# Kernel tuning notes

Hardware: AMD Instinct MI355X
Metric: run time of the kernel (lower is better)

## Reference

```python
import jax, jax.numpy as jnp
import numpy as np

N_NODES = 100000
N_EDGES = 2000000
EPS = 1e-8


def setup_inputs() -> dict:
    key = jax.random.key(0)
    k1, k2 = jax.random.split(key)
    node_positions = jax.random.normal(k1, (1, N_NODES, 2), dtype=jnp.float32) * 10.0
    adjacency = jnp.zeros((1, 1, 1), dtype=jnp.float32)  # unused by this axiom
    edge_index = jax.random.randint(k2, (2, N_EDGES), 0, N_NODES, dtype=jnp.int32)
    return {"node_positions": node_positions, "adjacency": adjacency, "edge_index": edge_index}


def reference(node_positions, adjacency, edge_index):
    """OrthogonalIntegrityAxiom loss.

    Mathematically identical to enumerating all intra-node edge pairs (i<j)
    and averaging cos^2(theta)*(1-cos^2(theta)) = dot^2 - dot^4 over pairs.
    Uses the moment identity: per node n with incident unit directions d_i,
      sum_{i,j} (d_i.d_j)^2 = ||sum_i d_i (x) d_i||_F^2
      sum_{i,j} (d_i.d_j)^4 = ||sum_i d_i^{(x)4}||_F^2
    Diagonal (i=j) terms equal 1 in both sums and cancel in the difference,
    so sum_{i<j} (dot^2 - dot^4) = (S2_n - S4_n)/2.
    """
    pos = node_positions.reshape(-1, 2)                      # (N, 2)
    n_total = pos.shape[0]
    src, dst = edge_index[0], edge_index[1]
    d = pos[dst] - pos[src]                                  # (E, 2)
    d = d / jnp.maximum(jnp.linalg.norm(d, axis=-1, keepdims=True), EPS)

    # Each edge is incident to both endpoints -> 2E (node, direction) pairs.
    nodes = jnp.concatenate([src, dst])                      # (2E,)
    dirs = jnp.concatenate([d, d], axis=0)                   # (2E, 2)

    o2 = (dirs[:, :, None] * dirs[:, None, :]).reshape(-1, 4)    # d (x) d, (2E, 4)
    o4 = (o2[:, :, None] * o2[:, None, :]).reshape(-1, 16)       # d^{(x)4}, (2E, 16)

    M = jax.ops.segment_sum(o2, nodes, num_segments=n_total)     # (N, 4)
    T = jax.ops.segment_sum(o4, nodes, num_segments=n_total)     # (N, 16)
    deg = jax.ops.segment_sum(jnp.ones_like(dirs[:, 0]), nodes, num_segments=n_total)

    S2 = jnp.sum(M * M, axis=-1)   # per-node sum_{i,j} (d_i.d_j)^2
    S4 = jnp.sum(T * T, axis=-1)   # per-node sum_{i,j} (d_i.d_j)^4

    pair_loss_sum = 0.5 * jnp.sum(S2 - S4)
    n_pairs = 0.5 * jnp.sum(deg * (deg - 1.0))
    loss = pair_loss_sum / jnp.maximum(n_pairs, 1.0)
    return loss
```

## Files before the change

### kernel.cpp

```cpp
#include <hip/hip_runtime.h>
#include <math.h>

#define EPSV 1e-8f

static constexpr double QC = 1.0 / 1024.0;
static constexpr double QS = 1.0 / 512.0;

static constexpr int BLOG = 8;
static constexpr int NPB = 1 << BLOG;
static constexpr int NBIN = 512;
static constexpr int SRTN = 8192;
static constexpr int NODE_BLOCKS = 256;

__device__ __forceinline__ unsigned int make_record(float dx, float dy) {
    float n2 = dx * dx + dy * dy;
    if (n2 > EPSV * EPSV) {
        float inv = 1.0f / n2;
        float c2 = (dx * dx - dy * dy) * inv;
        float s2 = (2.0f * dx * dy) * inv;
        float c4 = c2 * c2 - s2 * s2;
        float s4 = 2.0f * c2 * s2;
        c4 = fminf(fmaxf(c4, -1.0f), 1.0f);
        s4 = fminf(fmaxf(s4, -1.0f), 1.0f);
        unsigned int c4q = (unsigned int)__float2int_rn((c4 + 1.0f) * 1024.0f);
        unsigned int s4q = (unsigned int)__float2int_rn((s4 + 1.0f) * 512.0f);
        return (c4q << 11) | s4q;
    }
    return (1u << 31) | (1024u << 11) | 512u;
}

__device__ __forceinline__ unsigned long long rec_to_val(unsigned int r) {
    return (((unsigned long long)(r >> 31)) << 60) | (1ull << 52)
         | (((unsigned long long)((r >> 11) & 0xFFFu)) << 26)
         | (unsigned long long)(r & 0x7FFu);
}

__device__ __forceinline__ void decode_accum(unsigned long long a, double& pls, double& npr) {
    double s4sum = (double)(a & 0x3FFFFFFull);
    double c4sum = (double)((a >> 26) & 0x3FFFFFFull);
    double deg = (double)((a >> 52) & 0xFFull);
    double z = (double)(a >> 60);
    double u = deg - z;
    double C = c4sum * QC - deg;
    double S = s4sum * QS - deg;
    pls += (u * u - C * C - S * S) * 0.0625;
    npr += 0.5 * deg * (deg - 1.0);
}

__global__ __launch_bounds__(256) void bin_kernel(
    const float2* __restrict__ pos,
    const int* __restrict__ ei,
    int E, int NB, int chunk, int rstride,
    unsigned short* __restrict__ ofs_out,
    unsigned int* __restrict__ buf)
{
    __shared__ unsigned int srt[SRTN];
    __shared__ unsigned int hist[512];
    __shared__ unsigned int scan[512];
    int blk = blockIdx.x;
    int t = threadIdx.x;
    int e0 = blk * chunk;
    int e1 = min(E, e0 + chunk);
    int cl = max(0, e1 - e0);
    const int* src = ei;
    const int* dst = ei + E;

    hist[t] = 0; hist[t + 256] = 0;
    __syncthreads();
    for (int e = e0 + t; e < e1; e += 256) {
        atomicAdd(&hist[src[e] >> BLOG], 1u);
        atomicAdd(&hist[dst[e] >> BLOG], 1u);
    }
    __syncthreads();
    scan[t] = hist[t]; scan[t + 256] = hist[t + 256];
    __syncthreads();
    for (int d = 1; d < 512; d <<= 1) {
        unsigned a0 = scan[t] + ((t >= d) ? scan[t - d] : 0u);
        int t2 = t + 256;
        unsigned a1 = scan[t2] + ((t2 >= d) ? scan[t2 - d] : 0u);
        __syncthreads();
        scan[t] = a0; scan[t2] = a1;
        __syncthreads();
    }
    unsigned ex0 = scan[t] - hist[t];
    unsigned ex1 = scan[t + 256] - hist[t + 256];
    size_t row = (size_t)blk * (size_t)(NB + 1);
    if (t < NB) ofs_out[row + t] = (unsigned short)ex0;
    if (t + 256 < NB) ofs_out[row + t + 256] = (unsigned short)ex1;
    if (t == 0) ofs_out[row + NB] = (unsigned short)(2 * cl);
    __syncthreads();
    hist[t] = ex0; hist[t + 256] = ex1;
    __syncthreads();
    for (int e = e0 + t; e < e1; e += 256) {
        int s = src[e], d = dst[e];
        float2 ps = pos[s], pd = pos[d];
        unsigned int rec = make_record(pd.x - ps.x, pd.y - ps.y);
        unsigned is = atomicAdd(&hist[s >> BLOG], 1u);
        srt[is] = rec | ((unsigned)(s & (NPB - 1)) << 23);
        unsigned it = atomicAdd(&hist[d >> BLOG], 1u);
        srt[it] = rec | ((unsigned)(d & (NPB - 1)) << 23);
    }
    __syncthreads();
    unsigned int* dstb = buf + (size_t)blk * (size_t)rstride;
    int nrec = 2 * cl;
    for (int i = t; i < nrec; i += 256) dstb[i] = srt[i];
}

__global__ __launch_bounds__(512) void bucket_kernel(
    const unsigned int* __restrict__ buf,
    const unsigned short* __restrict__ ofs,
    int rstride, int NB, int nbin,
    double* __restrict__ partials)
{
    __shared__ unsigned long long acc[8][NPB];
    __shared__ unsigned int so0[NBIN], so1[NBIN];
    __shared__ double sha[8], shb[8];
    int b = blockIdx.x;
    int t = threadIdx.x;
    int wid = t >> 6;
    for (int i = t; i < 8 * NPB; i += 512)
        ((unsigned long long*)acc)[i] = 0ull;
    if (t < nbin) {
        size_t row = (size_t)t * (size_t)(NB + 1);
        so0[t] = ofs[row + b];
        so1[t] = ofs[row + b + 1];
    }
    __syncthreads();

    int g = t >> 4;
    int l = t & 15;
    for (int rr = g; rr < nbin; rr += 32) {
        unsigned o0 = so0[rr], o1 = so1[rr];
        const unsigned int* p = buf + (size_t)rr * (size_t)rstride;
        for (unsigned i = o0 + l; i < o1; i += 16) {
            unsigned r = p[i];
            unsigned id = (r >> 23) & (NPB - 1);
            atomicAdd(&acc[wid][id], rec_to_val(r));
        }
    }
    __syncthreads();

    double pls = 0.0, npr = 0.0;
    for (int i = t; i < NPB; i += 512) {
        unsigned long long a = 0ull;
        #pragma unroll
        for (int w = 0; w < 8; ++w) a += acc[w][i];
        decode_accum(a, pls, npr);
    }
    for (int off = 32; off > 0; off >>= 1) {
        pls += __shfl_down(pls, off, 64);
        npr += __shfl_down(npr, off, 64);
    }
    int lane = t & 63;
    if (lane == 0) { sha[wid] = pls; shb[wid] = npr; }
    __syncthreads();
    if (t == 0) {
        double a = 0.0, c = 0.0;
        #pragma unroll
        for (int w = 0; w < 8; ++w) { a += sha[w]; c += shb[w]; }
        partials[2 * b + 0] = a;
        partials[2 * b + 1] = c;
    }
}

__global__ __launch_bounds__(256) void final_kernel(
    const double* __restrict__ partials,
    float* __restrict__ out,
    int nb)
{
    double pls = 0.0, npr = 0.0;
    for (int i = threadIdx.x; i < nb; i += blockDim.x) {
        pls += partials[2 * i + 0];
        npr += partials[2 * i + 1];
    }
    __shared__ double sha[4], shb[4];
    for (int off = 32; off > 0; off >>= 1) {
        pls += __shfl_down(pls, off, 64);
        npr += __shfl_down(npr, off, 64);
    }
    int lane = threadIdx.x & 63;
    int wid = threadIdx.x >> 6;
    if (lane == 0) { sha[wid] = pls; shb[wid] = npr; }
    __syncthreads();
    if (threadIdx.x == 0) {
        double a = sha[0] + sha[1] + sha[2] + sha[3];
        double b = shb[0] + shb[1] + shb[2] + shb[3];
        out[0] = (float)(a / fmax(b, 1.0));
    }
}

__global__ __launch_bounds__(256) void edge_kernel_fb(
    const float2* __restrict__ pos,
    const int* __restrict__ ei,
    unsigned long long* __restrict__ acc,
    int E)
{
    int tid = blockIdx.x * blockDim.x + threadIdx.x;
    int nthreads = gridDim.x * blockDim.x;
    const int* src = ei;
    const int* dst = ei + E;
    for (int e = tid; e < E; e += nthreads) {
        int s = src[e], t = dst[e];
        float2 ps = pos[s], pt = pos[t];
        unsigned long long val = rec_to_val(make_record(pt.x - ps.x, pt.y - ps.y));
        atomicAdd(&acc[s], val);
        atomicAdd(&acc[t], val);
    }
}

__global__ __launch_bounds__(256) void node_kernel_fb(
    const unsigned long long* __restrict__ acc,
    double* __restrict__ partials,
    int N)
{
    int tid = blockIdx.x * blockDim.x + threadIdx.x;
    int nthreads = gridDim.x * blockDim.x;
    double pls = 0.0, npr = 0.0;
    for (int n = tid; n < N; n += nthreads)
        decode_accum(acc[n], pls, npr);
    __shared__ double sha[4], shb[4];
    for (int off = 32; off > 0; off >>= 1) {
        pls += __shfl_down(pls, off, 64);
        npr += __shfl_down(npr, off, 64);
    }
    int lane = threadIdx.x & 63;
    int wid = threadIdx.x >> 6;
    if (lane == 0) { sha[wid] = pls; shb[wid] = npr; }
    __syncthreads();
    if (threadIdx.x == 0) {
        partials[2 * blockIdx.x + 0] = sha[0] + sha[1] + sha[2] + sha[3];
        partials[2 * blockIdx.x + 1] = shb[0] + shb[1] + shb[2] + shb[3];
    }
}

extern "C" void kernel_launch(void* const* d_in, const int* in_sizes, int n_in,
                              void* d_out, int out_size, void* d_ws, size_t ws_size,
                              hipStream_t stream) {
    const float* pos = (const float*)d_in[0];
    const int* ei = (const int*)d_in[2];
    int N = in_sizes[0] / 2;
    int E = in_sizes[2] / 2;
    float* out = (float*)d_out;

    int NB = (N + NPB - 1) >> BLOG;
    int chunk = (E + NBIN - 1) / NBIN;
    int nrec_max = 2 * chunk;
    int rstride = (nrec_max + 15) & ~15;

    size_t off_buf = (size_t)NB * 16;
    size_t off_ofs = off_buf + (size_t)NBIN * (size_t)rstride * 4;
    size_t need = off_ofs + (size_t)NBIN * (size_t)(NB + 1) * 2;

    if (ws_size >= need && nrec_max <= SRTN && NB + 1 <= 512 && nrec_max < 65536) {
        double* partials = (double*)d_ws;
        unsigned int* buf = (unsigned int*)((char*)d_ws + off_buf);
        unsigned short* ofs = (unsigned short*)((char*)d_ws + off_ofs);

        bin_kernel<<<NBIN, 256, 0, stream>>>(
            (const float2*)pos, ei, E, NB, chunk, rstride, ofs, buf);
        bucket_kernel<<<NB, 512, 0, stream>>>(buf, ofs, rstride, NB, NBIN, partials);
        final_kernel<<<1, 256, 0, stream>>>(partials, out, NB);
    } else {
        unsigned long long* acc = (unsigned long long*)d_ws;
        double* partials = (double*)((char*)d_ws + (size_t)N * 8);
        hipMemsetAsync(d_ws, 0, (size_t)N * 8 + (size_t)NODE_BLOCKS * 16, stream);
        int eb = min((E + 255) / 256, 2048);
        edge_kernel_fb<<<eb, 256, 0, stream>>>((const float2*)pos, ei, acc, E);
        node_kernel_fb<<<NODE_BLOCKS, 256, 0, stream>>>(acc, partials, N);
        final_kernel<<<1, 256, 0, stream>>>(partials, out, NODE_BLOCKS);
    }
}
```

Measured before the change: 115.3 us.

## Compute edge records during histogram pass and fuse final reduction into bucket kernel

Edge direction records are now computed in the first histogram pass and kept in a shared-memory buffer, so the scatter pass no longer re-gathers positions. The final single-block reduction kernel is removed. Bucket blocks instead accumulate their partial sums with double atomics into a header that bin_kernel zeroes, and the last block to arrive writes the output. This saves a kernel launch and some redundant gathers, at the cost of extra LDS per block (which may lower occupancy), a non-deterministic summation order, and a last-block-done counter protocol.

```diff
diff --git a/kernel.cpp b/kernel.cpp
--- a/kernel.cpp
+++ b/kernel.cpp
@@ -10,6 +10,7 @@
 static constexpr int NPB = 1 << BLOG;
 static constexpr int NBIN = 512;
 static constexpr int SRTN = 8192;
+static constexpr int CHMAX = SRTN / 2;
 static constexpr int NODE_BLOCKS = 256;
 
 __device__ __forceinline__ unsigned int make_record(float dx, float dy) {
@@ -52,13 +53,16 @@
     const int* __restrict__ ei,
     int E, int NB, int chunk, int rstride,
     unsigned short* __restrict__ ofs_out,
-    unsigned int* __restrict__ buf)
+    unsigned int* __restrict__ buf,
+    unsigned long long* __restrict__ hdr)
 {
     __shared__ unsigned int srt[SRTN];
+    __shared__ unsigned int recbuf[CHMAX];
     __shared__ unsigned int hist[512];
     __shared__ unsigned int scan[512];
     int blk = blockIdx.x;
     int t = threadIdx.x;
+    if (blk == 0 && t < 4) hdr[t] = 0ull;
     int e0 = blk * chunk;
     int e1 = min(E, e0 + chunk);
     int cl = max(0, e1 - e0);
@@ -68,8 +72,11 @@
     hist[t] = 0; hist[t + 256] = 0;
     __syncthreads();
     for (int e = e0 + t; e < e1; e += 256) {
-        atomicAdd(&hist[src[e] >> BLOG], 1u);
-        atomicAdd(&hist[dst[e] >> BLOG], 1u);
+        int s = src[e], d = dst[e];
+        atomicAdd(&hist[s >> BLOG], 1u);
+        atomicAdd(&hist[d >> BLOG], 1u);
+        float2 ps = pos[s], pd = pos[d];
+        recbuf[e - e0] = make_record(pd.x - ps.x, pd.y - ps.y);
     }
     __syncthreads();
     scan[t] = hist[t]; scan[t + 256] = hist[t + 256];
@@ -93,8 +100,7 @@
     __syncthreads();
     for (int e = e0 + t; e < e1; e += 256) {
         int s = src[e], d = dst[e];
-        float2 ps = pos[s], pd = pos[d];
-        unsigned int rec = make_record(pd.x - ps.x, pd.y - ps.y);
+        unsigned int rec = recbuf[e - e0];
         unsigned is = atomicAdd(&hist[s >> BLOG], 1u);
         srt[is] = rec | ((unsigned)(s & (NPB - 1)) << 23);
         unsigned it = atomicAdd(&hist[d >> BLOG], 1u);
@@ -110,7 +116,8 @@
     const unsigned int* __restrict__ buf,
     const unsigned short* __restrict__ ofs,
     int rstride, int NB, int nbin,
-    double* __restrict__ partials)
+    unsigned long long* __restrict__ hdr,
+    float* __restrict__ out)
 {
     __shared__ unsigned long long acc[8][NPB];
     __shared__ unsigned int so0[NBIN], so1[NBIN];
@@ -158,8 +165,17 @@
         double a = 0.0, c = 0.0;
         #pragma unroll
         for (int w = 0; w < 8; ++w) { a += sha[w]; c += shb[w]; }
-        partials[2 * b + 0] = a;
-        partials[2 * b + 1] = c;
+        double* gs = (double*)hdr;
+        double r0 = atomicAdd(&gs[0], a);
+        double r1 = atomicAdd(&gs[1], c);
+        asm volatile("" :: "v"(r0), "v"(r1));
+        __threadfence();
+        unsigned long long cnt = atomicAdd(&hdr[2], 1ull);
+        if (cnt == (unsigned long long)(gridDim.x - 1)) {
+            double ta = atomicAdd(&gs[0], 0.0);
+            double tb = atomicAdd(&gs[1], 0.0);
+            out[0] = (float)(ta / fmax(tb, 1.0));
+        }
     }
 }
 
@@ -247,19 +263,18 @@
     int nrec_max = 2 * chunk;
     int rstride = (nrec_max + 15) & ~15;
 
-    size_t off_buf = (size_t)NB * 16;
+    size_t off_buf = 64;
     size_t off_ofs = off_buf + (size_t)NBIN * (size_t)rstride * 4;
     size_t need = off_ofs + (size_t)NBIN * (size_t)(NB + 1) * 2;
 
-    if (ws_size >= need && nrec_max <= SRTN && NB + 1 <= 512 && nrec_max < 65536) {
-        double* partials = (double*)d_ws;
+    if (ws_size >= need && chunk <= CHMAX && NB + 1 <= 512 && nrec_max < 65536) {
+        unsigned long long* hdr = (unsigned long long*)d_ws;
         unsigned int* buf = (unsigned int*)((char*)d_ws + off_buf);
         unsigned short* ofs = (unsigned short*)((char*)d_ws + off_ofs);
 
         bin_kernel<<<NBIN, 256, 0, stream>>>(
-            (const float2*)pos, ei, E, NB, chunk, rstride, ofs, buf);
-        bucket_kernel<<<NB, 512, 0, stream>>>(buf, ofs, rstride, NB, NBIN, partials);
-        final_kernel<<<1, 256, 0, stream>>>(partials, out, NB);
+            (const float2*)pos, ei, E, NB, chunk, rstride, ofs, buf, hdr);
+        bucket_kernel<<<NB, 512, 0, stream>>>(buf, ofs, rstride, NB, NBIN, hdr, out);
     } else {
         unsigned long long* acc = (unsigned long long*)d_ws;
         double* partials = (double*)((char*)d_ws + (size_t)N * 8);
```

Result: slower. 122.5 us (+6.3%).

## Stage edge indices in LDS with vectorized loads and widen bin kernel to 512 threads

Applied to the files above, without the earlier changes.

The bin kernel now reads each block's edge indices once with int4 loads into LDS (sdu/sdv) and builds its histogram from them. The scatter pass reuses these staged indices instead of re-reading global memory. Block size goes from 256 to 512 threads, the scan becomes one element per thread, and the final copy-out uses uint4 stores. The chunk is rounded to a multiple of 8 for alignment, and LDS use grows by 32KB per block, which may lower occupancy.

```diff
diff --git a/kernel.cpp b/kernel.cpp
--- a/kernel.cpp
+++ b/kernel.cpp
@@ -10,6 +10,7 @@
 static constexpr int NPB = 1 << BLOG;
 static constexpr int NBIN = 512;
 static constexpr int SRTN = 8192;
+static constexpr int SDMAX = 4096;
 static constexpr int NODE_BLOCKS = 256;
 
 __device__ __forceinline__ unsigned int make_record(float dx, float dy) {
@@ -47,14 +48,16 @@
     npr += 0.5 * deg * (deg - 1.0);
 }
 
-__global__ __launch_bounds__(256) void bin_kernel(
+__global__ __launch_bounds__(512) void bin_kernel(
     const float2* __restrict__ pos,
     const int* __restrict__ ei,
     int E, int NB, int chunk, int rstride,
     unsigned short* __restrict__ ofs_out,
     unsigned int* __restrict__ buf)
 {
-    __shared__ unsigned int srt[SRTN];
+    __shared__ __align__(16) unsigned int srt[SRTN];
+    __shared__ __align__(16) int sdu[SDMAX];
+    __shared__ __align__(16) int sdv[SDMAX];
     __shared__ unsigned int hist[512];
     __shared__ unsigned int scan[512];
     int blk = blockIdx.x;
@@ -62,37 +65,53 @@
     int e0 = blk * chunk;
     int e1 = min(E, e0 + chunk);
     int cl = max(0, e1 - e0);
-    const int* src = ei;
-    const int* dst = ei + E;
-
-    hist[t] = 0; hist[t + 256] = 0;
-    __syncthreads();
-    for (int e = e0 + t; e < e1; e += 256) {
-        atomicAdd(&hist[src[e] >> BLOG], 1u);
-        atomicAdd(&hist[dst[e] >> BLOG], 1u);
-    }
-    __syncthreads();
-    scan[t] = hist[t]; scan[t + 256] = hist[t + 256];
+    const int* src = ei + e0;
+    const int* dst = ei + E + e0;
+
+    hist[t] = 0;
+    __syncthreads();
+    if (((E & 3) == 0)) {
+        int nq = cl >> 2;
+        for (int q = t; q < nq; q += 512) {
+            int4 s4 = ((const int4*)src)[q];
+            int4 d4 = ((const int4*)dst)[q];
+            ((int4*)sdu)[q] = s4;
+            ((int4*)sdv)[q] = d4;
+            atomicAdd(&hist[s4.x >> BLOG], 1u);
+            atomicAdd(&hist[s4.y >> BLOG], 1u);
+            atomicAdd(&hist[s4.z >> BLOG], 1u);
+            atomicAdd(&hist[s4.w >> BLOG], 1u);
+            atomicAdd(&hist[d4.x >> BLOG], 1u);
+            atomicAdd(&hist[d4.y >> BLOG], 1u);
+            atomicAdd(&hist[d4.z >> BLOG], 1u);
+            atomicAdd(&hist[d4.w >> BLOG], 1u);
+        }
+    } else {
+        for (int i = t; i < cl; i += 512) {
+            int s = src[i], d = dst[i];
+            sdu[i] = s; sdv[i] = d;
+            atomicAdd(&hist[s >> BLOG], 1u);
+            atomicAdd(&hist[d >> BLOG], 1u);
+        }
+    }
+    __syncthreads();
+    scan[t] = hist[t];
     __syncthreads();
     for (int d = 1; d < 512; d <<= 1) {
-        unsigned a0 = scan[t] + ((t >= d) ? scan[t - d] : 0u);
-        int t2 = t + 256;
-        unsigned a1 = scan[t2] + ((t2 >= d) ? scan[t2 - d] : 0u);
+        unsigned a = scan[t] + ((t >= d) ? scan[t - d] : 0u);
         __syncthreads();
-        scan[t] = a0; scan[t2] = a1;
+        scan[t] = a;
         __syncthreads();
     }
-    unsigned ex0 = scan[t] - hist[t];
-    unsigned ex1 = scan[t + 256] - hist[t + 256];
+    unsigned ex = scan[t] - hist[t];
     size_t row = (size_t)blk * (size_t)(NB + 1);
-    if (t < NB) ofs_out[row + t] = (unsigned short)ex0;
-    if (t + 256 < NB) ofs_out[row + t + 256] = (unsigned short)ex1;
+    if (t < NB) ofs_out[row + t] = (unsigned short)ex;
     if (t == 0) ofs_out[row + NB] = (unsigned short)(2 * cl);
     __syncthreads();
-    hist[t] = ex0; hist[t + 256] = ex1;
-    __syncthreads();
-    for (int e = e0 + t; e < e1; e += 256) {
-        int s = src[e], d = dst[e];
+    hist[t] = ex;
+    __syncthreads();
+    for (int i = t; i < cl; i += 512) {
+        int s = sdu[i], d = sdv[i];
         float2 ps = pos[s], pd = pos[d];
         unsigned int rec = make_record(pd.x - ps.x, pd.y - ps.y);
         unsigned is = atomicAdd(&hist[s >> BLOG], 1u);
@@ -103,7 +122,13 @@
     __syncthreads();
     unsigned int* dstb = buf + (size_t)blk * (size_t)rstride;
     int nrec = 2 * cl;
-    for (int i = t; i < nrec; i += 256) dstb[i] = srt[i];
+    if ((nrec & 3) == 0) {
+        int nv = nrec >> 2;
+        for (int i = t; i < nv; i += 512)
+            ((uint4*)dstb)[i] = ((const uint4*)srt)[i];
+    } else {
+        for (int i = t; i < nrec; i += 512) dstb[i] = srt[i];
+    }
 }
 
 __global__ __launch_bounds__(512) void bucket_kernel(
@@ -243,7 +268,7 @@
     float* out = (float*)d_out;
 
     int NB = (N + NPB - 1) >> BLOG;
-    int chunk = (E + NBIN - 1) / NBIN;
+    int chunk = ((E + NBIN - 1) / NBIN + 7) & ~7;
     int nrec_max = 2 * chunk;
     int rstride = (nrec_max + 15) & ~15;
 
@@ -251,12 +276,13 @@
     size_t off_ofs = off_buf + (size_t)NBIN * (size_t)rstride * 4;
     size_t need = off_ofs + (size_t)NBIN * (size_t)(NB + 1) * 2;
 
-    if (ws_size >= need && nrec_max <= SRTN && NB + 1 <= 512 && nrec_max < 65536) {
+    if (ws_size >= need && chunk <= SDMAX && nrec_max <= SRTN
+        && NB + 1 <= 512 && nrec_max < 65536) {
         double* partials = (double*)d_ws;
         unsigned int* buf = (unsigned int*)((char*)d_ws + off_buf);
         unsigned short* ofs = (unsigned short*)((char*)d_ws + off_ofs);
 
-        bin_kernel<<<NBIN, 256, 0, stream>>>(
+        bin_kernel<<<NBIN, 512, 0, stream>>>(
             (const float2*)pos, ei, E, NB, chunk, rstride, ofs, buf);
         bucket_kernel<<<NB, 512, 0, stream>>>(buf, ofs, rstride, NB, NBIN, partials);
         final_kernel<<<1, 256, 0, stream>>>(partials, out, NB);
```

Measured after the change: 107.0 us, median of 2. 7.2% less time.
